# Performance work log

Hardware: AMD Instinct MI355X
Metric: run time of the kernel (lower is better)

## Reference

```python
import math
import jax, jax.numpy as jnp
import numpy as np

IMG = 512; P = 16; CIN = 3; COUT = 3; E = 768; NHEADS = 12; L = 8
NPH = IMG // P            # 32 patches per side
N = NPH * NPH             # 1024 tokens (must match learned 1024x1024 attn bias)
HD = E // NHEADS          # 64
INTER = min(E // 2, 128)  # 128, OutputProjection intermediate
EPS = 1e-5


def _sin_pe(n_h, n_w, d):
    # faithful port of get_2d_sinusoidal_encoding (second half stays zero)
    pe = np.zeros((n_h, n_w, d), dtype=np.float32)
    dq, dh = d // 4, d // 2
    div = np.exp(np.arange(0, dq, 2, dtype=np.float32) * (-math.log(10000.0) / dq))
    pr = np.arange(n_h, dtype=np.float32)[:, None]
    pc = np.arange(n_w, dtype=np.float32)[:, None]
    pe[:, :, 0:dq:2] = np.sin(pr * div)[:, None, :]
    pe[:, :, 1:dq:2] = np.cos(pr * div)[:, None, :]
    pe[:, :, dq:dh:2] = np.sin(pc * div)[None, :, :]
    pe[:, :, dq + 1:dh:2] = np.cos(pc * div)[None, :, :]
    return jnp.asarray(pe.reshape(-1, d))


def _ln(x, g, b):
    m = x.mean(-1, keepdims=True)
    v = ((x - m) ** 2).mean(-1, keepdims=True)
    return (x - m) * jax.lax.rsqrt(v + EPS) * g + b


def setup_inputs():
    key = jax.random.key(0)
    ks = iter(jax.random.split(key, 32))
    def nrm(shape, scale=0.02):
        return jax.random.normal(next(ks), shape, jnp.float32) * scale
    return {
        'x': jax.random.normal(next(ks), (2, CIN, IMG, IMG), jnp.float32),
        'conv_w': nrm((E, CIN, P, P)), 'conv_b': jnp.zeros((E,), jnp.float32),
        'ln1_g': jnp.ones((L, E), jnp.float32), 'ln1_b': jnp.zeros((L, E), jnp.float32),
        'qkv_w': nrm((L, 3 * E, E)),
        'proj_w': nrm((L, E, E)), 'proj_b': jnp.zeros((L, E), jnp.float32),
        'attn_bias': jax.random.normal(next(ks), (L, N, N), jnp.float32),  # torch.randn init
        'ln2_g': jnp.ones((L, E), jnp.float32), 'ln2_b': jnp.zeros((L, E), jnp.float32),
        'mlp_w1': nrm((L, 2 * E, E)), 'mlp_b1': jnp.zeros((L, 2 * E), jnp.float32),
        'mlp_w2': nrm((L, E, 2 * E)), 'mlp_b2': jnp.zeros((L, E), jnp.float32),
        'op_w1': nrm((INTER, E)), 'op_b1': jnp.zeros((INTER,), jnp.float32),
        'op_w2': nrm((P * P * COUT, INTER)), 'op_b2': jnp.zeros((P * P * COUT,), jnp.float32),
        'ag_wg': nrm((1, COUT), 0.2), 'ag_bng_w': jnp.ones((), jnp.float32), 'ag_bng_b': jnp.zeros((), jnp.float32),
        'ag_wx': nrm((1, CIN), 0.2), 'ag_bnx_w': jnp.ones((), jnp.float32), 'ag_bnx_b': jnp.zeros((), jnp.float32),
        'ag_psi_w': jnp.full((), 0.5, jnp.float32), 'ag_psi_b': jnp.zeros((), jnp.float32),
    }


def reference(x, conv_w, conv_b, ln1_g, ln1_b, qkv_w, proj_w, proj_b, attn_bias,
              ln2_g, ln2_b, mlp_w1, mlp_b1, mlp_w2, mlp_b2,
              op_w1, op_b1, op_w2, op_b2,
              ag_wg, ag_bng_w, ag_bng_b, ag_wx, ag_bnx_w, ag_bnx_b, ag_psi_w, ag_psi_b):
    B = x.shape[0]
    # --- VisionTransformerInput: patch-embed conv (stride == kernel) as reshape+GEMM ---
    xp = x.reshape(B, CIN, NPH, P, NPH, P).transpose(0, 2, 4, 1, 3, 5).reshape(B, N, CIN * P * P)
    t = xp @ conv_w.reshape(E, -1).T + conv_b
    t = t + _sin_pe(NPH, NPH, E)[None]

    # --- encoder blocks (scan over stacked per-layer params) ---
    def block(t, p):
        y = _ln(t, p['ln1_g'], p['ln1_b'])
        qkv = (y @ p['qkv_w'].T).reshape(B, N, 3, NHEADS, HD).transpose(2, 0, 3, 1, 4)
        q, k, v = qkv[0], qkv[1], qkv[2]
        s = jnp.einsum('bhnd,bhmd->bhnm', q, k) / math.sqrt(HD)
        # NOTE: relative_position_bias is computed but never added in the source (dead code);
        # only the learned (N,N) bias parameter is added.
        s = s + p['attn_bias'][None, None]
        a = jax.nn.softmax(s, axis=-1)
        o = jnp.einsum('bhnm,bhmd->bhnd', a, v).transpose(0, 2, 1, 3).reshape(B, N, E)
        o = o @ p['proj_w'].T + p['proj_b']
        t = t + (y + o)  # MHA has an extra internal residual (out = x + out) in the source
        h = _ln(t, p['ln2_g'], p['ln2_b'])
        h = jax.nn.gelu(h @ p['mlp_w1'].T + p['mlp_b1'], approximate=False) @ p['mlp_w2'].T + p['mlp_b2']
        return t + h, None

    stacked = {'ln1_g': ln1_g, 'ln1_b': ln1_b, 'qkv_w': qkv_w, 'proj_w': proj_w,
               'proj_b': proj_b, 'attn_bias': attn_bias, 'ln2_g': ln2_g, 'ln2_b': ln2_b,
               'mlp_w1': mlp_w1, 'mlp_b1': mlp_b1, 'mlp_w2': mlp_w2, 'mlp_b2': mlp_b2}
    t, _ = jax.lax.scan(block, t, stacked)

    # --- OutputProjection: MLP -> Fold -> attention gate -> (identity) interpolate ---
    h = jax.nn.relu(t @ op_w1.T + op_b1) @ op_w2.T + op_b2  # (B, N, C*P*P)
    # nn.Fold(kernel=stride=P): columns interpreted as (C, P, P)
    g = h.reshape(B, NPH, NPH, COUT, P, P).transpose(0, 3, 1, 4, 2, 5).reshape(B, COUT, IMG, IMG)
    inv = 1.0 / math.sqrt(1.0 + EPS)  # BatchNorm eval: running_mean=0, running_var=1
    g1 = jnp.einsum('bchw,oc->bohw', g, ag_wg) * (inv * ag_bng_w) + ag_bng_b
    x1 = jnp.einsum('bchw,oc->bohw', x, ag_wx) * (inv * ag_bnx_w) + ag_bnx_b
    psi = jax.nn.sigmoid(jax.nn.relu(g1 + x1) * ag_psi_w + ag_psi_b)
    out = g * (x * psi)  # x * att_gate's psi == skip_gated; then x_fold * skip_gated
    # F.interpolate to (output_size, output_size) with output_size == image_size: identity
    return out
```

## Files before the change

kernel.cpp:

```cpp
#include <hip/hip_runtime.h>
#include <math.h>

typedef unsigned short u16;
typedef unsigned int u32;
typedef __attribute__((ext_vector_type(8))) short bf16x8;
typedef __attribute__((ext_vector_type(16))) float f32x16;
typedef __attribute__((ext_vector_type(4))) float f4v;
typedef __attribute__((ext_vector_type(4))) u32 u32x4;

#define MFMA(a, b, c) __builtin_amdgcn_mfma_f32_32x32x16_bf16(a, b, c, 0, 0, 0)

#define SYNC_STEP() do {                                   \
    asm volatile("s_waitcnt vmcnt(0)" ::: "memory");       \
    __builtin_amdgcn_s_barrier();                          \
    __builtin_amdgcn_sched_barrier(0);                     \
} while (0)

#define SYNC_CNT6() do {                                   \
    asm volatile("s_waitcnt vmcnt(6)" ::: "memory");       \
    __builtin_amdgcn_s_barrier();                          \
    __builtin_amdgcn_sched_barrier(0);                     \
} while (0)

__device__ __forceinline__ float bf2f(u16 h) { return __uint_as_float(((u32)h) << 16); }

__device__ __forceinline__ void split2(float v, u16& h, u16& l) {
    u32 u = __float_as_uint(v);
    u32 hr = (u + 0x7FFFu + ((u >> 16) & 1u)) & 0xFFFF0000u;
    h = (u16)(hr >> 16);
    float lf = v - __uint_as_float(hr);
    u32 ul = __float_as_uint(lf);
    l = (u16)((ul + 0x7FFFu + ((ul >> 16) & 1u)) >> 16);
}

__device__ __forceinline__ u32 cvtpk(float lo, float hi) {
    u32 r;
    asm("v_cvt_pk_bf16_f32 %0, %1, %2" : "=v"(r) : "v"(lo), "v"(hi));
    return r;
}

__device__ __forceinline__ void swap32(u32& a, u32& b, int hi) {
    u32 ta = (u32)__shfl_xor((int)a, 32);
    u32 tb = (u32)__shfl_xor((int)b, 32);
    u32 na = hi ? tb : a;
    u32 nb = hi ? b : ta;
    a = na; b = nb;
}

__device__ __forceinline__ void repack(const f32x16& v, int base, int hi, bf16x8& fh, bf16x8& fl) {
    float p0 = v[base + 0], p1 = v[base + 1], p2 = v[base + 2], p3 = v[base + 3];
    float p4 = v[base + 4], p5 = v[base + 5], p6 = v[base + 6], p7 = v[base + 7];
    u32 X0 = cvtpk(p0, p1), X1 = cvtpk(p2, p3), X4 = cvtpk(p4, p5), X5 = cvtpk(p6, p7);
    float r0 = p0 - __uint_as_float(X0 << 16);
    float r1 = p1 - __uint_as_float(X0 & 0xFFFF0000u);
    float r2 = p2 - __uint_as_float(X1 << 16);
    float r3 = p3 - __uint_as_float(X1 & 0xFFFF0000u);
    float r4 = p4 - __uint_as_float(X4 << 16);
    float r5 = p5 - __uint_as_float(X4 & 0xFFFF0000u);
    float r6 = p6 - __uint_as_float(X5 << 16);
    float r7 = p7 - __uint_as_float(X5 & 0xFFFF0000u);
    u32 L0 = cvtpk(r0, r1), L1 = cvtpk(r2, r3), L4 = cvtpk(r4, r5), L5 = cvtpk(r6, r7);
    swap32(X0, X4, hi); swap32(X1, X5, hi);
    swap32(L0, L4, hi); swap32(L1, L5, hi);
    u32x4 th = {X0, X1, X4, X5};
    u32x4 tl = {L0, L1, L4, L5};
    fh = __builtin_bit_cast(bf16x8, th);
    fl = __builtin_bit_cast(bf16x8, tl);
}

__global__ __launch_bounds__(256) void pe_kernel(float* __restrict__ pe) {
    int idx = blockIdx.x * 256 + threadIdx.x;
    int n = idx / 768, d = idx - n * 768;
    float v = 0.0f;
    if (d < 384) {
// ... 46 lines not shown
    else if (idx < 2359296) { src = projw; off = idx - 1769472; }
    else if (idx < 3538944) { src = w1;    off = idx - 2359296; }
    else                    { src = w2;    off = idx - 3538944; }
    float4 v = *(const float4*)(src + off);
    split2(v.x, wh[idx], wl[idx]);
    split2(v.y, wh[idx + 1], wl[idx + 1]);
    split2(v.z, wh[idx + 2], wl[idx + 2]);
    split2(v.w, wh[idx + 3], wl[idx + 3]);
}

__global__ __launch_bounds__(256) void btrans(const float* __restrict__ src, float* __restrict__ dst) {
    __shared__ float tl[32][33];
    int bx = blockIdx.x & 31, by = blockIdx.x >> 5;
    int tx = threadIdx.x & 31, ty = threadIdx.x >> 5;
#pragma unroll
    for (int j = 0; j < 4; ++j)
        tl[ty + j * 8][tx] = src[(size_t)(by * 32 + ty + j * 8) * 1024 + bx * 32 + tx];
    __syncthreads();
#pragma unroll
    for (int j = 0; j < 4; ++j)
        dst[(size_t)(bx * 32 + ty + j * 8) * 1024 + by * 32 + tx] = tl[tx][ty + j * 8];
}

__global__ __launch_bounds__(256) void ln_kernel(const float* __restrict__ x,
                                                 const float* __restrict__ g,
                                                 const float* __restrict__ b,
                                                 u16* __restrict__ yh, u16* __restrict__ yl) {
    int row = blockIdx.x, tid = threadIdx.x;
    int wid = tid >> 6, lane = tid & 63;
    const float* xr = x + (size_t)row * 768;
    float v0 = xr[tid], v1 = xr[tid + 256], v2 = xr[tid + 512];
    __shared__ float ws[8];
    float sum = v0 + v1 + v2;
#pragma unroll
    for (int off = 32; off > 0; off >>= 1) sum += __shfl_xor(sum, off);
    if (lane == 0) ws[wid] = sum;
    __syncthreads();
    float mean = (ws[0] + ws[1] + ws[2] + ws[3]) * (1.0f / 768.0f);
    float d0 = v0 - mean, d1 = v1 - mean, d2 = v2 - mean;
    float vs = d0 * d0 + d1 * d1 + d2 * d2;
#pragma unroll
    for (int off = 32; off > 0; off >>= 1) vs += __shfl_xor(vs, off);
    if (lane == 0) ws[4 + wid] = vs;
    __syncthreads();
    float rstd = rsqrtf((ws[4] + ws[5] + ws[6] + ws[7]) * (1.0f / 768.0f) + 1e-5f);
    size_t o = (size_t)row * 768;
    split2(d0 * rstd * g[tid]       + b[tid],       yh[o + tid],       yl[o + tid]);
    split2(d1 * rstd * g[tid + 256] + b[tid + 256], yh[o + tid + 256], yl[o + tid + 256]);
    split2(d2 * rstd * g[tid + 512] + b[tid + 512], yh[o + tid + 512], yl[o + tid + 512]);
}

__device__ __forceinline__ int mrow(int r) { return (r + (r >> 2)) & 3; }

template <int MODE>
__global__ __launch_bounds__(256, 2) void gemm_sp(const u16* __restrict__ Ah, const u16* __restrict__ Al,
                                                  const u16* __restrict__ Bh, const u16* __restrict__ Bl,
                                                  const float* __restrict__ bias,
                                                  const float* __restrict__ res,
                                                  const float* __restrict__ auxf,
                                                  const u16* __restrict__ auxh, const u16* __restrict__ auxl,
                                                  float* __restrict__ C, u16* __restrict__ Ch, u16* __restrict__ Cl,
                                                  u16* __restrict__ Cth, u16* __restrict__ Ctl,
                                                  int M, int N, int K, int nby) {
    __shared__ u16 SH[36864];
    u16* As = SH;
    u16* Bs = SH + 12288;
    int tid = threadIdx.x;
    int wid = tid >> 6, lane = tid & 63;
    int hi = lane >> 5;
    int lq = lane & 31;
    int wm = wid >> 1, wn = wid & 1;

    int nwg = gridDim.x;
    int q8 = nwg >> 3;
    int swz = (blockIdx.x & 7) * q8 + (blockIdx.x >> 3);
    int cb = swz / nby, rb = swz - cb * nby;
    int m0 = rb * 64, n0 = cb * 128;

    f32x16 acc0 = {}, acc1 = {};

    auto stage = [&](int buf, int kt) {
#pragma unroll
        for (int c = 0; c < 2; ++c) {
            const u16* G = c ? Al : Ah;
            int row = wid * 16 + (lane >> 2);
            int ch = (lane & 3) ^ mrow(row);
            const u16* g = G + (size_t)(m0 + row) * K + kt + ch * 8;
            __builtin_amdgcn_global_load_lds((const __attribute__((address_space(1))) u32*)g,
                                             (__attribute__((address_space(3))) u32*)&As[(buf * 2 + c) * 2048 + (wid * 16) * 32],
                                             16, 0, 0);
        }
#pragma unroll
        for (int c = 0; c < 2; ++c) {
            const u16* G = c ? Bl : Bh;
#pragma unroll
            for (int j = 0; j < 2; ++j) {
                int row = wid * 32 + j * 16 + (lane >> 2);
                int ch = (lane & 3) ^ mrow(row);
                const u16* g = G + (size_t)(n0 + row) * K + kt + ch * 8;
                __builtin_amdgcn_global_load_lds((const __attribute__((address_space(1))) u32*)g,
                                                 (__attribute__((address_space(3))) u32*)&Bs[(buf * 2 + c) * 4096 + (wid * 32 + j * 16) * 32],
                                                 16, 0, 0);
            }
        }
    };

    int ar  = wm * 32 + lq;
    int br0 = wn * 64 + lq;
    int br1 = br0 + 32;

    auto compute = [&](int buf) {
#pragma unroll
        for (int kc = 0; kc < 2; ++kc) {
            int gc = (kc << 1) | hi;
            int oA  = ar  * 32 + ((gc ^ mrow(ar))  << 3);
            int oB0 = br0 * 32 + ((gc ^ mrow(br0)) << 3);
            int oB1 = br1 * 32 + ((gc ^ mrow(br1)) << 3);
            bf16x8 ah  = *(const bf16x8*)(As + (buf * 2 + 0) * 2048 + oA);
            bf16x8 al  = *(const bf16x8*)(As + (buf * 2 + 1) * 2048 + oA);
            bf16x8 b0h = *(const bf16x8*)(Bs + (buf * 2 + 0) * 4096 + oB0);
            bf16x8 b0l = *(const bf16x8*)(Bs + (buf * 2 + 1) * 4096 + oB0);
            bf16x8 b1h = *(const bf16x8*)(Bs + (buf * 2 + 0) * 4096 + oB1);
            bf16x8 b1l = *(const bf16x8*)(Bs + (buf * 2 + 1) * 4096 + oB1);
            acc0 = MFMA(ah, b0h, acc0);
            acc0 = MFMA(ah, b0l, acc0);
            acc0 = MFMA(al, b0h, acc0);
            acc1 = MFMA(ah, b1h, acc1);
            acc1 = MFMA(ah, b1l, acc1);
            acc1 = MFMA(al, b1h, acc1);
        }
    };

    int nk = K >> 5;
    stage(0, 0);
    stage(1, 32);
    int t = 0;
    for (; t < nk - 1; ++t) {
        SYNC_CNT6();
        if (t + 2 < nk) stage((t + 2) % 3, (t + 2) << 5);
        compute(t % 3);
    }
    SYNC_STEP();
    compute(t % 3);

    if (MODE == 7 && n0 >= 1536) {
        __syncthreads();
        auto scatterV = [&](const f32x16& a, int fn) {
            int c = wn * 64 + fn * 32 + lq;
            int rb2 = wm * 32 + (hi << 2);
#pragma unroll
            for (int r = 0; r < 16; ++r) {
                int rr = rb2 + (r & 3) + ((r >> 2) << 3);
                u16 hv, lv;
                split2(a[r], hv, lv);
                SH[c * 68 + rr] = hv;
                SH[8704 + c * 68 + rr] = lv;
            }
        };
        scatterV(acc0, 0);
        scatterV(acc1, 1);
        __syncthreads();
        int bb = m0 >> 10;
        int nbase = m0 & 1023;
#pragma unroll
        for (int pass = 0; pass < 4; ++pass) {
            int c2 = pass * 32 + (tid >> 3);
            int ch8 = tid & 7;
            int hcol = (n0 - 1536) + c2;
            int h2 = hcol >> 6, hd = hcol & 63;
            size_t dst = ((size_t)(bb * 12 + h2) * 64 + hd) * 1024 + nbase + ch8 * 8;
            int so = c2 * 68 + ch8 * 8;
            u32x4 ph = {*(const u32*)&SH[so], *(const u32*)&SH[so + 2],
                        *(const u32*)&SH[so + 4], *(const u32*)&SH[so + 6]};
            u32x4 pl = {*(const u32*)&SH[8704 + so], *(const u32*)&SH[8704 + so + 2],
                        *(const u32*)&SH[8704 + so + 4], *(const u32*)&SH[8704 + so + 6]};
            *(u32x4*)(Cth + dst) = ph;
            *(u32x4*)(Ctl + dst) = pl;
        }
        return;
    }

    auto epi = [&](const f32x16& a, int fn) {
        int col = n0 + wn * 64 + fn * 32 + lq;
        int rb2 = m0 + wm * 32 + (hi << 2);
#pragma unroll
        for (int r = 0; r < 16; ++r) {
            int row = rb2 + (r & 3) + ((r >> 2) << 3);
            float v = a[r];
            size_t o = (size_t)row * N + col;
            if (MODE == 1) C[o] = v + bias[col] + auxf[(size_t)(row & 1023) * N + col];
            else if (MODE == 2) C[o] = res[o] + (bf2f(auxh[o]) + bf2f(auxl[o])) + v + bias[col];
            else if (MODE == 3) {
                v += bias[col];
                v = 0.5f * v * (1.0f + erff(v * 0.70710678118654752f));
                split2(v, Ch[o], Cl[o]);
            }
            else if (MODE == 4) C[o] = res[o] + v + bias[col];
            else if (MODE == 5) {
                v += bias[col];
                v = fmaxf(v, 0.0f);
                split2(v, Ch[o], Cl[o]);
            }
            else if (MODE == 6) C[o] = v + bias[col];
            else if (MODE == 7) {
                size_t o7 = (size_t)row * 1536 + col;
                split2(v, Ch[o7], Cl[o7]);
            }
        }
    };
    epi(acc0, 0); epi(acc1, 1);
}

__global__ __launch_bounds__(256, 2) void attn_mfma(const u16* __restrict__ qh, const u16* __restrict__ ql,
                                                    const u16* __restrict__ vth, const u16* __restrict__ vtl,
                                                    const float* __restrict__ biasT,
                                                    u16* __restrict__ oh, u16* __restrict__ ol) {
    __shared__ u16 smem[2][2][4][2048];
    int tid = threadIdx.x;
    int wid = tid >> 6, lane = tid & 63;
    int s = wid & 1, p = wid >> 1;
    int lq = lane & 31;
    int hi = lane >> 5;
    int id = blockIdx.x;
    int xcd = id & 7;
    int j = id >> 3;
    int bh = xcd * 3 + (j >> 4);
    int qt = j & 15;
    int b = bh / 12, h = bh % 12;
    int bq0 = qt * 64;
    int gq = bq0 + s * 32 + lq;

    bf16x8 qfh[4], qfl[4];
    {
        size_t qo = (size_t)(b * 1024 + gq) * 1536 + h * 64 + hi * 8;
#pragma unroll
        for (int ks = 0; ks < 4; ++ks) {
            qfh[ks] = *(const bf16x8*)(qh + qo + ks * 16);
            qfl[ks] = *(const bf16x8*)(ql + qo + ks * 16);
        }
    }

    f32x16 oa = {}, ob = {};
    float m_i = -1e30f, l_i = 0.0f;

    auto stage = [&](int buf, int kb) {
        if (s == 0) {
#pragma unroll
            for (int c = 0; c < 2; ++c) {
                const u16* G = c ? ql : qh;
#pragma unroll
                for (int i = 0; i < 4; ++i) {
                    int r = 8 * i + (lane >> 3);
                    int cl = (lane & 7) ^ (r & 7);
                    const u16* g = G + (size_t)(b * 1024 + kb + r) * 1536 + 768 + h * 64 + cl * 8;
                    __builtin_amdgcn_global_load_lds((const __attribute__((address_space(1))) u32*)g,
                                                     (__attribute__((address_space(3))) u32*)&smem[p][buf][c][i * 512],
                                                     16, 0, 0);
                }
            }
        } else {
#pragma unroll
            for (int c = 0; c < 2; ++c) {
                const u16* G = c ? vtl : vth;
#pragma unroll
                for (int i = 0; i < 4; ++i) {
                    int r = 16 * i + (lane >> 2);
                    int cl = (lane & 3) ^ ((r >> 1) & 3);
                    const u16* g = G + ((size_t)(b * 12 + h) * 64 + r) * 1024 + kb + cl * 8;
                    __builtin_amdgcn_global_load_lds((const __attribute__((address_space(1))) u32*)g,
                                                     (__attribute__((address_space(3))) u32*)&smem[p][buf][2 + c][i * 512],
                                                     16, 0, 0);
                }
            }
        }
    };

    auto loadBias = [&](float (&bb)[16], int kb) {
        const float* bbase = biasT + (size_t)(kb + 4 * hi) * 1024 + gq;
#pragma unroll
        for (int g2 = 0; g2 < 4; ++g2)
#pragma unroll
            for (int q = 0; q < 4; ++q)
                bb[g2 * 4 + q] = bbase[(size_t)(g2 * 8 + q) * 1024];
    };

    auto compute = [&](int buf, const float (&bb)[16]) {
        const u16* Kh = &smem[p][buf][0][0];
        const u16* Kl = &smem[p][buf][1][0];
        const u16* Vh = &smem[p][buf][2][0];
        const u16* Vl = &smem[p][buf][3][0];
        f32x16 s0 = {}, s1 = {};
        __builtin_amdgcn_s_setprio(1);
#pragma unroll
        for (int ks = 0; ks < 2; ++ks) {
            int offA = lq * 64 + (((2 * ks + hi) ^ (lq & 7)) << 3);
            int offB = lq * 64 + (((2 * (ks + 2) + hi) ^ (lq & 7)) << 3);
            bf16x8 khA = *(const bf16x8*)(Kh + offA);
            bf16x8 klA = *(const bf16x8*)(Kl + offA);
            bf16x8 khB = *(const bf16x8*)(Kh + offB);
            bf16x8 klB = *(const bf16x8*)(Kl + offB);
            s0 = MFMA(khA, qfh[ks], s0);
            s1 = MFMA(khB, qfh[ks + 2], s1);
            s0 = MFMA(khA, qfl[ks], s0);
            s1 = MFMA(khB, qfl[ks + 2], s1);
            s0 = MFMA(klA, qfh[ks], s0);
            s1 = MFMA(klB, qfh[ks + 2], s1);
        }
        __builtin_amdgcn_s_setprio(0);
        bf16x8 vf[2][4];
#pragma unroll
        for (int kslot = 0; kslot < 2; ++kslot) {
            int offa = lq * 32 + (((2 * kslot + hi) ^ ((lq >> 1) & 3)) << 3);
            vf[kslot][0] = *(const bf16x8*)(Vh + offa);
            vf[kslot][1] = *(const bf16x8*)(Vh + offa + 1024);
            vf[kslot][2] = *(const bf16x8*)(Vl + offa);
            vf[kslot][3] = *(const bf16x8*)(Vl + offa + 1024);
        }
        f32x16 sa;
#pragma unroll
        for (int r = 0; r < 16; ++r) sa[r] = (s0[r] + s1[r]) * 0.125f + bb[r];
        float m01 = fmaxf(sa[0], sa[1]),  m23 = fmaxf(sa[2], sa[3]);
        float m45 = fmaxf(sa[4], sa[5]),  m67 = fmaxf(sa[6], sa[7]);
        float m89 = fmaxf(sa[8], sa[9]),  mab = fmaxf(sa[10], sa[11]);
        float mcd = fmaxf(sa[12], sa[13]), mef = fmaxf(sa[14], sa[15]);
        float pm = fmaxf(fmaxf(fmaxf(m01, m23), fmaxf(m45, m67)),
                         fmaxf(fmaxf(m89, mab), fmaxf(mcd, mef)));
        pm = fmaxf(pm, __shfl_xor(pm, 32));
        if (__any(pm > m_i + 8.0f)) {
            float mnew = fmaxf(m_i, pm);
            float scl = __expf(m_i - mnew);
            m_i = mnew;
            l_i *= scl;
#pragma unroll
            for (int r = 0; r < 16; ++r) {
                int qr = (r & 3) + 8 * (r >> 2) + 4 * hi;
                float fr = __shfl(scl, qr);
                oa[r] *= fr; ob[r] *= fr;
            }
        }
        float ls = 0.0f;
#pragma unroll
        for (int r = 0; r < 16; ++r) { sa[r] = __expf(sa[r] - m_i); ls += sa[r]; }
        ls += __shfl_xor(ls, 32);
        l_i += ls;
        __builtin_amdgcn_s_setprio(1);
#pragma unroll
        for (int kslot = 0; kslot < 2; ++kslot) {
            bf16x8 ph, pl;
            repack(sa, kslot * 8, hi, ph, pl);
            oa = MFMA(ph, vf[kslot][0], oa);
            oa = MFMA(ph, vf[kslot][2], oa);
            oa = MFMA(pl, vf[kslot][0], oa);
            ob = MFMA(ph, vf[kslot][1], ob);
            ob = MFMA(ph, vf[kslot][3], ob);
            ob = MFMA(pl, vf[kslot][1], ob);
        }
        __builtin_amdgcn_s_setprio(0);
    };

    float bbA[16], bbB[16];
    stage(0, p * 32);
    loadBias(bbA, p * 32);
    for (int ss = 0; ss < 16; ss += 2) {
        SYNC_STEP();
        if (ss + 1 < 16) { stage(1, (2 * (ss + 1) + p) * 32); loadBias(bbB, (2 * (ss + 1) + p) * 32); }
        compute(0, bbA);
        SYNC_STEP();
        if (ss + 2 < 16) { stage(0, (2 * (ss + 2) + p) * 32); loadBias(bbA, (2 * (ss + 2) + p) * 32); }
        compute(1, bbB);
    }
    __syncthreads();

    float* mlb = (float*)((char*)smem + 32768);
    mlb[((s * 2 + p) * 2 + 0) * 32 + lq] = m_i;
    mlb[((s * 2 + p) * 2 + 1) * 32 + lq] = l_i;
    __syncthreads();
    float mo  = mlb[((s * 2 + (p ^ 1)) * 2 + 0) * 32 + lq];
    float lo_ = mlb[((s * 2 + (p ^ 1)) * 2 + 1) * 32 + lq];
    float M = fmaxf(m_i, mo);
    float ea = __expf(m_i - M), eb = __expf(mo - M);
    float L = ea * l_i + eb * lo_;
    float f = ea / L;
    float frv[16];
#pragma unroll
    for (int r = 0; r < 16; ++r) frv[r] = __shfl(f, (r & 3) + 8 * (r >> 2) + 4 * hi);
    float* ox = (float*)((char*)smem + s * 8192);
    if (p == 1) {
#pragma unroll
        for (int r = 0; r < 16; ++r) {
            int qr = (r & 3) + 8 * (r >> 2) + 4 * hi;
            ox[qr * 64 + lq] = oa[r] * frv[r];
            ox[qr * 64 + 32 + lq] = ob[r] * frv[r];
        }
    }
    __syncthreads();
    if (p == 0) {
#pragma unroll
        for (int r = 0; r < 16; ++r) {
            int qr = (r & 3) + 8 * (r >> 2) + 4 * hi;
            float va = oa[r] * frv[r] + ox[qr * 64 + lq];
            float vb = ob[r] * frv[r] + ox[qr * 64 + 32 + lq];
            size_t d = (size_t)(b * 1024 + bq0 + s * 32 + qr) * 768 + h * 64;
            split2(va, oh[d + lq], ol[d + lq]);
            split2(vb, oh[d + 32 + lq], ol[d + 32 + lq]);
        }
    }
}

__global__ __launch_bounds__(256) void fold_gate(const float* __restrict__ hbuf,
                                                 const float* __restrict__ xin,
                                                 const float* __restrict__ wg,
                                                 const float* __restrict__ bngw,
                                                 const float* __restrict__ bngb,
                                                 const float* __restrict__ wx,
                                                 const float* __restrict__ bnxw,
                                                 const float* __restrict__ bnxb,
                                                 const float* __restrict__ psiw,
                                                 const float* __restrict__ psib,
                                                 float* __restrict__ out) {
    int idx = blockIdx.x * 256 + threadIdx.x;
// ... 24 lines not shown
    const float* x       = (const float*)d_in[0];
    const float* conv_w  = (const float*)d_in[1];
    const float* conv_b  = (const float*)d_in[2];
    const float* ln1_g   = (const float*)d_in[3];
    const float* ln1_b   = (const float*)d_in[4];
    const float* qkv_w   = (const float*)d_in[5];
    const float* proj_w  = (const float*)d_in[6];
    const float* proj_b  = (const float*)d_in[7];
    const float* attn_bs = (const float*)d_in[8];
    const float* ln2_g   = (const float*)d_in[9];
    const float* ln2_b   = (const float*)d_in[10];
    const float* mlp_w1  = (const float*)d_in[11];
    const float* mlp_b1  = (const float*)d_in[12];
    const float* mlp_w2  = (const float*)d_in[13];
    const float* mlp_b2  = (const float*)d_in[14];
    const float* op_w1   = (const float*)d_in[15];
    const float* op_b1   = (const float*)d_in[16];
    const float* op_w2   = (const float*)d_in[17];
    const float* op_b2   = (const float*)d_in[18];
    const float* ag_wg   = (const float*)d_in[19];
    const float* ag_bngw = (const float*)d_in[20];
    const float* ag_bngb = (const float*)d_in[21];
    const float* ag_wx   = (const float*)d_in[22];
    const float* ag_bnxw = (const float*)d_in[23];
    const float* ag_bnxb = (const float*)d_in[24];
    const float* ag_psiw = (const float*)d_in[25];
    const float* ag_psib = (const float*)d_in[26];
    float* out = (float*)d_out;

    char* w8 = (char*)d_ws;
    float* t     = (float*)(w8);
    u16* yh      = (u16*)(w8 + 6291456);
    u16* yl      = (u16*)(w8 + 9437184);
    u16* ath     = (u16*)(w8 + 12582912);
    u16* atl     = (u16*)(w8 + 15728640);
    u16* mh      = (u16*)(w8 + 18874368);
    u16* ml      = (u16*)(w8 + 25165824);
    u16* qh      = (u16*)(w8 + 31457280);
    u16* ql      = (u16*)(w8 + 37748736);
    u16* wh      = (u16*)(w8 + 44040192);
    u16* wl      = (u16*)(w8 + 53477376);
    float* biasT = (float*)(w8 + 62914560);
    float* pe  = (float*)qh;
    u16* xph = mh; u16* xpl = ml;
    u16* vth = mh; u16* vtl = ml;
    float* oph2 = (float*)qh;
    u16* o1h = ath; u16* o1l = atl;

    const size_t W_QKV = 0, W_PROJ = 1769472, W_MLP1 = 2359296, W_MLP2 = 3538944;

    pe_kernel<<<3072, 256, 0, stream>>>(pe);
    gather_kernel<<<6144, 256, 0, stream>>>(x, xph, xpl);
    fsplit<<<576, 256, 0, stream>>>(conv_w, wh, wl, 147456);
    gemm_sp<1><<<192, 256, 0, stream>>>(xph, xpl, wh, wl, conv_b, nullptr, pe,
                                        nullptr, nullptr, t, nullptr, nullptr,
                                        nullptr, nullptr, 2048, 768, 768, 32);

    for (int l = 0; l < 8; ++l) {
        wsplit_layer<<<4608, 256, 0, stream>>>(qkv_w + (size_t)l * 1769472, proj_w + (size_t)l * 589824,
                                               mlp_w1 + (size_t)l * 1179648, mlp_w2 + (size_t)l * 1179648,
                                               wh, wl);
        btrans<<<1024, 256, 0, stream>>>(attn_bs + (size_t)l * 1048576, biasT);
        ln_kernel<<<2048, 256, 0, stream>>>(t, ln1_g + l * 768, ln1_b + l * 768, yh, yl);
        gemm_sp<7><<<576, 256, 0, stream>>>(yh, yl, wh + W_QKV, wl + W_QKV, nullptr, nullptr,
                                            nullptr, nullptr, nullptr, nullptr, qh, ql,
                                            vth, vtl, 2048, 2304, 768, 32);
        attn_mfma<<<384, 256, 0, stream>>>(qh, ql, vth, vtl, biasT, ath, atl);
        gemm_sp<2><<<192, 256, 0, stream>>>(ath, atl, wh + W_PROJ, wl + W_PROJ, proj_b + l * 768,
                                            t, nullptr, yh, yl, t, nullptr, nullptr,
                                            nullptr, nullptr, 2048, 768, 768, 32);
        ln_kernel<<<2048, 256, 0, stream>>>(t, ln2_g + l * 768, ln2_b + l * 768, yh, yl);
        gemm_sp<3><<<384, 256, 0, stream>>>(yh, yl, wh + W_MLP1, wl + W_MLP1, mlp_b1 + l * 1536,
                                            nullptr, nullptr, nullptr, nullptr, nullptr, mh, ml,
                                            nullptr, nullptr, 2048, 1536, 768, 32);
        gemm_sp<4><<<192, 256, 0, stream>>>(mh, ml, wh + W_MLP2, wl + W_MLP2, mlp_b2 + l * 768,
                                            t, nullptr, nullptr, nullptr, t, nullptr, nullptr,
                                            nullptr, nullptr, 2048, 768, 1536, 32);
    }

    fsplit<<<1536, 256, 0, stream>>>(t, yh, yl, 393216);
    fsplit<<<96, 256, 0, stream>>>(op_w1, wh, wl, 24576);
    fsplit<<<96, 256, 0, stream>>>(op_w2, wh + 131072, wl + 131072, 24576);
    gemm_sp<5><<<32, 256, 0, stream>>>(yh, yl, wh, wl, op_b1, nullptr, nullptr,
                                       nullptr, nullptr, nullptr, o1h, o1l,
                                       nullptr, nullptr, 2048, 128, 768, 32);
    gemm_sp<6><<<192, 256, 0, stream>>>(o1h, o1l, wh + 131072, wl + 131072, op_b2, nullptr,
                                        nullptr, nullptr, nullptr, oph2, nullptr, nullptr,
                                        nullptr, nullptr, 2048, 768, 128, 32);
    fold_gate<<<2048, 256, 0, stream>>>(oph2, x, ag_wg, ag_bngw, ag_bngb,
                                        ag_wx, ag_bnxw, ag_bnxb, ag_psiw, ag_psib, out);
}
```

Baseline: 1.427 ms.

## Add 32-row GEMM tile variant, re-layout V staging, relax attention barrier waits

```diff
diff --git a/kernel.cpp b/kernel.cpp
--- a/kernel.cpp
+++ b/kernel.cpp
@@ -16,10 +16,10 @@
     __builtin_amdgcn_sched_barrier(0);                     \
 } while (0)
 
-#define SYNC_CNT6() do {                                   \
-    asm volatile("s_waitcnt vmcnt(6)" ::: "memory");       \
-    __builtin_amdgcn_s_barrier();                          \
-    __builtin_amdgcn_sched_barrier(0);                     \
+#define SYNC_CNT_LIT(nlit) do {                                    \
+    asm volatile("s_waitcnt vmcnt(" #nlit ")" ::: "memory");       \
+    __builtin_amdgcn_s_barrier();                                  \
+    __builtin_amdgcn_sched_barrier(0);                             \
 } while (0)
 
 __device__ __forceinline__ float bf2f(u16 h) { return __uint_as_float(((u32)h) << 16); }
@@ -172,7 +172,7 @@
 
 __device__ __forceinline__ int mrow(int r) { return (r + (r >> 2)) & 3; }
 
-template <int MODE>
+template <int MODE, int BM>
 __global__ __launch_bounds__(256, 2) void gemm_sp(const u16* __restrict__ Ah, const u16* __restrict__ Al,
                                                   const u16* __restrict__ Bh, const u16* __restrict__ Bl,
                                                   const float* __restrict__ bias,
@@ -182,32 +182,42 @@
                                                   float* __restrict__ C, u16* __restrict__ Ch, u16* __restrict__ Cl,
                                                   u16* __restrict__ Cth, u16* __restrict__ Ctl,
                                                   int M, int N, int K, int nby) {
-    __shared__ u16 SH[36864];
+    constexpr int ABUF = BM * 32;
+    __shared__ u16 SH[6 * ABUF + 24576];
     u16* As = SH;
-    u16* Bs = SH + 12288;
+    u16* Bs = SH + 6 * ABUF;
     int tid = threadIdx.x;
     int wid = tid >> 6, lane = tid & 63;
     int hi = lane >> 5;
     int lq = lane & 31;
-    int wm = wid >> 1, wn = wid & 1;
 
     int nwg = gridDim.x;
     int q8 = nwg >> 3;
     int swz = (blockIdx.x & 7) * q8 + (blockIdx.x >> 3);
     int cb = swz / nby, rb = swz - cb * nby;
-    int m0 = rb * 64, n0 = cb * 128;
+    int m0 = rb * BM, n0 = cb * 128;
 
     f32x16 acc0 = {}, acc1 = {};
 
     auto stage = [&](int buf, int kt) {
-#pragma unroll
-        for (int c = 0; c < 2; ++c) {
-            const u16* G = c ? Al : Ah;
-            int row = wid * 16 + (lane >> 2);
+        if constexpr (BM == 64) {
+#pragma unroll
+            for (int c = 0; c < 2; ++c) {
+                const u16* G = c ? Al : Ah;
+                int row = wid * 16 + (lane >> 2);
+                int ch = (lane & 3) ^ mrow(row);
+                const u16* g = G + (size_t)(m0 + row) * K + kt + ch * 8;
+                __builtin_amdgcn_global_load_lds((const __attribute__((address_space(1))) u32*)g,
+                                                 (__attribute__((address_space(3))) u32*)&As[(buf * 2 + c) * ABUF + (wid * 16) * 32],
+                                                 16, 0, 0);
+            }
+        } else {
+            const u16* G = (wid & 1) ? Al : Ah;
+            int row = (wid >> 1) * 16 + (lane >> 2);
             int ch = (lane & 3) ^ mrow(row);
             const u16* g = G + (size_t)(m0 + row) * K + kt + ch * 8;
             __builtin_amdgcn_global_load_lds((const __attribute__((address_space(1))) u32*)g,
-                                             (__attribute__((address_space(3))) u32*)&As[(buf * 2 + c) * 2048 + (wid * 16) * 32],
+                                             (__attribute__((address_space(3))) u32*)&As[(buf * 2 + (wid & 1)) * ABUF + ((wid >> 1) * 16) * 32],
                                              16, 0, 0);
         }
 #pragma unroll
@@ -225,8 +235,8 @@
         }
     };
 
-    int ar  = wm * 32 + lq;
-    int br0 = wn * 64 + lq;
+    int ar  = (BM == 64) ? ((wid >> 1) * 32 + lq) : lq;
+    int br0 = (BM == 64) ? ((wid & 1) * 64 + lq) : (wid * 32 + lq);
     int br1 = br0 + 32;
 
     auto compute = [&](int buf) {
@@ -235,19 +245,21 @@
             int gc = (kc << 1) | hi;
             int oA  = ar  * 32 + ((gc ^ mrow(ar))  << 3);
             int oB0 = br0 * 32 + ((gc ^ mrow(br0)) << 3);
-            int oB1 = br1 * 32 + ((gc ^ mrow(br1)) << 3);
-            bf16x8 ah  = *(const bf16x8*)(As + (buf * 2 + 0) * 2048 + oA);
-            bf16x8 al  = *(const bf16x8*)(As + (buf * 2 + 1) * 2048 + oA);
+            bf16x8 ah  = *(const bf16x8*)(As + (buf * 2 + 0) * ABUF + oA);
+            bf16x8 al  = *(const bf16x8*)(As + (buf * 2 + 1) * ABUF + oA);
             bf16x8 b0h = *(const bf16x8*)(Bs + (buf * 2 + 0) * 4096 + oB0);
             bf16x8 b0l = *(const bf16x8*)(Bs + (buf * 2 + 1) * 4096 + oB0);
-            bf16x8 b1h = *(const bf16x8*)(Bs + (buf * 2 + 0) * 4096 + oB1);
-            bf16x8 b1l = *(const bf16x8*)(Bs + (buf * 2 + 1) * 4096 + oB1);
             acc0 = MFMA(ah, b0h, acc0);
             acc0 = MFMA(ah, b0l, acc0);
             acc0 = MFMA(al, b0h, acc0);
-            acc1 = MFMA(ah, b1h, acc1);
-            acc1 = MFMA(ah, b1l, acc1);
-            acc1 = MFMA(al, b1h, acc1);
+            if constexpr (BM == 64) {
+                int oB1 = br1 * 32 + ((gc ^ mrow(br1)) << 3);
+                bf16x8 b1h = *(const bf16x8*)(Bs + (buf * 2 + 0) * 4096 + oB1);
+                bf16x8 b1l = *(const bf16x8*)(Bs + (buf * 2 + 1) * 4096 + oB1);
+                acc1 = MFMA(ah, b1h, acc1);
+                acc1 = MFMA(ah, b1l, acc1);
+                acc1 = MFMA(al, b1h, acc1);
+            }
         }
     };
 
@@ -256,53 +268,55 @@
     stage(1, 32);
     int t = 0;
     for (; t < nk - 1; ++t) {
-        SYNC_CNT6();
+        if constexpr (BM == 64) SYNC_CNT_LIT(6); else SYNC_CNT_LIT(5);
         if (t + 2 < nk) stage((t + 2) % 3, (t + 2) << 5);
         compute(t % 3);
     }
     SYNC_STEP();
     compute(t % 3);
 
-    if (MODE == 7 && n0 >= 1536) {
-        __syncthreads();
-        auto scatterV = [&](const f32x16& a, int fn) {
-            int c = wn * 64 + fn * 32 + lq;
-            int rb2 = wm * 32 + (hi << 2);
-#pragma unroll
-            for (int r = 0; r < 16; ++r) {
-                int rr = rb2 + (r & 3) + ((r >> 2) << 3);
-                u16 hv, lv;
-                split2(a[r], hv, lv);
-                SH[c * 68 + rr] = hv;
-                SH[8704 + c * 68 + rr] = lv;
-            }
-        };
-        scatterV(acc0, 0);
-        scatterV(acc1, 1);
-        __syncthreads();
-        int bb = m0 >> 10;
-        int nbase = m0 & 1023;
-#pragma unroll
-        for (int pass = 0; pass < 4; ++pass) {
-            int c2 = pass * 32 + (tid >> 3);
-            int ch8 = tid & 7;
-            int hcol = (n0 - 1536) + c2;
-            int h2 = hcol >> 6, hd = hcol & 63;
-            size_t dst = ((size_t)(bb * 12 + h2) * 64 + hd) * 1024 + nbase + ch8 * 8;
-            int so = c2 * 68 + ch8 * 8;
-            u32x4 ph = {*(const u32*)&SH[so], *(const u32*)&SH[so + 2],
-                        *(const u32*)&SH[so + 4], *(const u32*)&SH[so + 6]};
-            u32x4 pl = {*(const u32*)&SH[8704 + so], *(const u32*)&SH[8704 + so + 2],
-                        *(const u32*)&SH[8704 + so + 4], *(const u32*)&SH[8704 + so + 6]};
-            *(u32x4*)(Cth + dst) = ph;
-            *(u32x4*)(Ctl + dst) = pl;
-        }
-        return;
-    }
-
-    auto epi = [&](const f32x16& a, int fn) {
-        int col = n0 + wn * 64 + fn * 32 + lq;
-        int rb2 = m0 + wm * 32 + (hi << 2);
+    if constexpr (MODE == 7) {
+        if (n0 >= 1536) {
+            __syncthreads();
+            auto scatterV = [&](const f32x16& a, int fn) {
+                int c = (wid & 1) * 64 + fn * 32 + lq;
+                int rb2 = (wid >> 1) * 32 + (hi << 2);
+#pragma unroll
+                for (int r = 0; r < 16; ++r) {
+                    int rr = rb2 + (r & 3) + ((r >> 2) << 3);
+                    u16 hv, lv;
+                    split2(a[r], hv, lv);
+                    SH[c * 68 + rr] = hv;
+                    SH[8704 + c * 68 + rr] = lv;
+                }
+            };
+            scatterV(acc0, 0);
+            scatterV(acc1, 1);
+            __syncthreads();
+            int bb = m0 >> 10;
+            int nbase = m0 & 1023;
+#pragma unroll
+            for (int pass = 0; pass < 4; ++pass) {
+                int c2 = pass * 32 + (tid >> 3);
+                int ch8 = tid & 7;
+                int hcol = (n0 - 1536) + c2;
+                int h2 = hcol >> 6, hd = hcol & 63;
+                size_t dst = ((size_t)(bb * 12 + h2) * 64 + hd) * 1024 + nbase + ch8 * 8;
+                int so = c2 * 68 + ch8 * 8;
+                u32x4 ph = {*(const u32*)&SH[so], *(const u32*)&SH[so + 2],
+                            *(const u32*)&SH[so + 4], *(const u32*)&SH[so + 6]};
+                u32x4 pl = {*(const u32*)&SH[8704 + so], *(const u32*)&SH[8704 + so + 2],
+                            *(const u32*)&SH[8704 + so + 4], *(const u32*)&SH[8704 + so + 6]};
+                *(u32x4*)(Cth + dst) = ph;
+                *(u32x4*)(Ctl + dst) = pl;
+            }
+            return;
+        }
+    }
+
+    auto epi = [&](const f32x16& a, int ncol) {
+        int col = n0 + ncol + lq;
+        int rb2 = m0 + ((BM == 64) ? ((wid >> 1) * 32) : 0) + (hi << 2);
 #pragma unroll
         for (int r = 0; r < 16; ++r) {
             int row = rb2 + (r & 3) + ((r >> 2) << 3);
@@ -328,7 +342,12 @@
             }
         }
     };
-    epi(acc0, 0); epi(acc1, 1);
+    if constexpr (BM == 64) {
+        epi(acc0, (wid & 1) * 64);
+        epi(acc1, (wid & 1) * 64 + 32);
+    } else {
+        epi(acc0, wid * 32);
+    }
 }
 
 __global__ __launch_bounds__(256, 2) void attn_mfma(const u16* __restrict__ qh, const u16* __restrict__ ql,
@@ -349,6 +368,7 @@
     int b = bh / 12, h = bh % 12;
     int bq0 = qt * 64;
     int gq = bq0 + s * 32 + lq;
+    size_t vbase = (size_t)(b * 12 + h) * 65536;
 
     bf16x8 qfh[4], qfl[4];
     {
@@ -384,9 +404,12 @@
                 const u16* G = c ? vtl : vth;
 #pragma unroll
                 for (int i = 0; i < 4; ++i) {
-                    int r = 16 * i + (lane >> 2);
-                    int cl = (lane & 3) ^ ((r >> 1) & 3);
-                    const u16* g = G + ((size_t)(b * 12 + h) * 64 + r) * 1024 + kb + cl * 8;
+                    int r = 8 * i + (lane >> 3);
+                    int pc = lane & 7;
+                    int lc = pc ^ (r & 7);
+                    int hd = r + ((lc >> 2) << 5);
+                    int kc = lc & 3;
+                    const u16* g = G + vbase + (size_t)hd * 1024 + kb + kc * 8;
                     __builtin_amdgcn_global_load_lds((const __attribute__((address_space(1))) u32*)g,
                                                      (__attribute__((address_space(3))) u32*)&smem[p][buf][2 + c][i * 512],
                                                      16, 0, 0);
@@ -430,11 +453,13 @@
         bf16x8 vf[2][4];
 #pragma unroll
         for (int kslot = 0; kslot < 2; ++kslot) {
-            int offa = lq * 32 + (((2 * kslot + hi) ^ ((lq >> 1) & 3)) << 3);
-            vf[kslot][0] = *(const bf16x8*)(Vh + offa);
-            vf[kslot][1] = *(const bf16x8*)(Vh + offa + 1024);
-            vf[kslot][2] = *(const bf16x8*)(Vl + offa);
-            vf[kslot][3] = *(const bf16x8*)(Vl + offa + 1024);
+            int ks2 = 2 * kslot + hi;
+            int off0 = lq * 64 + ((ks2 ^ (lq & 7)) << 3);
+            int off1 = lq * 64 + (((4 + ks2) ^ (lq & 7)) << 3);
+            vf[kslot][0] = *(const bf16x8*)(Vh + off0);
+            vf[kslot][1] = *(const bf16x8*)(Vh + off1);
+            vf[kslot][2] = *(const bf16x8*)(Vl + off0);
+            vf[kslot][3] = *(const bf16x8*)(Vl + off1);
         }
         f32x16 sa;
 #pragma unroll
@@ -482,10 +507,10 @@
     stage(0, p * 32);
     loadBias(bbA, p * 32);
     for (int ss = 0; ss < 16; ss += 2) {
-        SYNC_STEP();
+        SYNC_CNT_LIT(16);
         if (ss + 1 < 16) { stage(1, (2 * (ss + 1) + p) * 32); loadBias(bbB, (2 * (ss + 1) + p) * 32); }
         compute(0, bbA);
-        SYNC_STEP();
+        SYNC_CNT_LIT(16);
         if (ss + 2 < 16) { stage(0, (2 * (ss + 2) + p) * 32); loadBias(bbA, (2 * (ss + 2) + p) * 32); }
         compute(1, bbB);
     }
@@ -616,9 +641,9 @@
     pe_kernel<<<3072, 256, 0, stream>>>(pe);
     gather_kernel<<<6144, 256, 0, stream>>>(x, xph, xpl);
     fsplit<<<576, 256, 0, stream>>>(conv_w, wh, wl, 147456);
-    gemm_sp<1><<<192, 256, 0, stream>>>(xph, xpl, wh, wl, conv_b, nullptr, pe,
-                                        nullptr, nullptr, t, nullptr, nullptr,
-                                        nullptr, nullptr, 2048, 768, 768, 32);
+    gemm_sp<1, 32><<<384, 256, 0, stream>>>(xph, xpl, wh, wl, conv_b, nullptr, pe,
+                                            nullptr, nullptr, t, nullptr, nullptr,
+                                            nullptr, nullptr, 2048, 768, 768, 64);
 
     for (int l = 0; l < 8; ++l) {
         wsplit_layer<<<4608, 256, 0, stream>>>(qkv_w + (size_t)l * 1769472, proj_w + (size_t)l * 589824,
@@ -626,31 +651,31 @@
                                                wh, wl);
         btrans<<<1024, 256, 0, stream>>>(attn_bs + (size_t)l * 1048576, biasT);
         ln_kernel<<<2048, 256, 0, stream>>>(t, ln1_g + l * 768, ln1_b + l * 768, yh, yl);
-        gemm_sp<7><<<576, 256, 0, stream>>>(yh, yl, wh + W_QKV, wl + W_QKV, nullptr, nullptr,
-                                            nullptr, nullptr, nullptr, nullptr, qh, ql,
-                                            vth, vtl, 2048, 2304, 768, 32);
+        gemm_sp<7, 64><<<576, 256, 0, stream>>>(yh, yl, wh + W_QKV, wl + W_QKV, nullptr, nullptr,
+                                                nullptr, nullptr, nullptr, nullptr, qh, ql,
+                                                vth, vtl, 2048, 2304, 768, 32);
         attn_mfma<<<384, 256, 0, stream>>>(qh, ql, vth, vtl, biasT, ath, atl);
-        gemm_sp<2><<<192, 256, 0, stream>>>(ath, atl, wh + W_PROJ, wl + W_PROJ, proj_b + l * 768,
-                                            t, nullptr, yh, yl, t, nullptr, nullptr,
-                                            nullptr, nullptr, 2048, 768, 768, 32);
+        gemm_sp<2, 32><<<384, 256, 0, stream>>>(ath, atl, wh + W_PROJ, wl + W_PROJ, proj_b + l * 768,
+                                                t, nullptr, yh, yl, t, nullptr, nullptr,
+                                                nullptr, nullptr, 2048, 768, 768, 64);
         ln_kernel<<<2048, 256, 0, stream>>>(t, ln2_g + l * 768, ln2_b + l * 768, yh, yl);
-        gemm_sp<3><<<384, 256, 0, stream>>>(yh, yl, wh + W_MLP1, wl + W_MLP1, mlp_b1 + l * 1536,
-                                            nullptr, nullptr, nullptr, nullptr, nullptr, mh, ml,
-                                            nullptr, nullptr, 2048, 1536, 768, 32);
-        gemm_sp<4><<<192, 256, 0, stream>>>(mh, ml, wh + W_MLP2, wl + W_MLP2, mlp_b2 + l * 768,
-                                            t, nullptr, nullptr, nullptr, t, nullptr, nullptr,
-                                            nullptr, nullptr, 2048, 768, 1536, 32);
+        gemm_sp<3, 64><<<384, 256, 0, stream>>>(yh, yl, wh + W_MLP1, wl + W_MLP1, mlp_b1 + l * 1536,
+                                                nullptr, nullptr, nullptr, nullptr, nullptr, mh, ml,
+                                                nullptr, nullptr, 2048, 1536, 768, 32);
+        gemm_sp<4, 32><<<384, 256, 0, stream>>>(mh, ml, wh + W_MLP2, wl + W_MLP2, mlp_b2 + l * 768,
+                                                t, nullptr, nullptr, nullptr, t, nullptr, nullptr,
+                                                nullptr, nullptr, 2048, 768, 1536, 64);
     }
 
     fsplit<<<1536, 256, 0, stream>>>(t, yh, yl, 393216);
     fsplit<<<96, 256, 0, stream>>>(op_w1, wh, wl, 24576);
     fsplit<<<96, 256, 0, stream>>>(op_w2, wh + 131072, wl + 131072, 24576);
-    gemm_sp<5><<<32, 256, 0, stream>>>(yh, yl, wh, wl, op_b1, nullptr, nullptr,
-                                       nullptr, nullptr, nullptr, o1h, o1l,
-                                       nullptr, nullptr, 2048, 128, 768, 32);
-    gemm_sp<6><<<192, 256, 0, stream>>>(o1h, o1l, wh + 131072, wl + 131072, op_b2, nullptr,
-                                        nullptr, nullptr, nullptr, oph2, nullptr, nullptr,
-                                        nullptr, nullptr, 2048, 768, 128, 32);
+    gemm_sp<5, 32><<<64, 256, 0, stream>>>(yh, yl, wh, wl, op_b1, nullptr, nullptr,
+                                           nullptr, nullptr, nullptr, o1h, o1l,
+                                           nullptr, nullptr, 2048, 128, 768, 64);
+    gemm_sp<6, 32><<<384, 256, 0, stream>>>(o1h, o1l, wh + 131072, wl + 131072, op_b2, nullptr,
+                                            nullptr, nullptr, nullptr, oph2, nullptr, nullptr,
+                                            nullptr, nullptr, 2048, 768, 128, 64);
     fold_gate<<<2048, 256, 0, stream>>>(oph2, x, ag_wg, ag_bngw, ag_bngb,
                                         ag_wx, ag_bnxw, ag_bnxb, ag_psiw, ag_psib, out);
 }
```

Measured after the change: 1.520 ms. +6.5%, slower.

## Add 128x128-tile split-bf16 GEMM for QKV and MLP1 projections

Applied to the files above, without the earlier changes.

```diff
diff --git a/kernel.cpp b/kernel.cpp
--- a/kernel.cpp
+++ b/kernel.cpp
@@ -16,10 +16,10 @@
     __builtin_amdgcn_sched_barrier(0);                     \
 } while (0)
 
-#define SYNC_CNT6() do {                                   \
-    asm volatile("s_waitcnt vmcnt(6)" ::: "memory");       \
-    __builtin_amdgcn_s_barrier();                          \
-    __builtin_amdgcn_sched_barrier(0);                     \
+#define SYNC_CNT_LIT(nlit) do {                                    \
+    asm volatile("s_waitcnt vmcnt(" #nlit ")" ::: "memory");       \
+    __builtin_amdgcn_s_barrier();                                  \
+    __builtin_amdgcn_sched_barrier(0);                             \
 } while (0)
 
 __device__ __forceinline__ float bf2f(u16 h) { return __uint_as_float(((u32)h) << 16); }
@@ -180,7 +180,6 @@
                                                   const float* __restrict__ auxf,
                                                   const u16* __restrict__ auxh, const u16* __restrict__ auxl,
                                                   float* __restrict__ C, u16* __restrict__ Ch, u16* __restrict__ Cl,
-                                                  u16* __restrict__ Cth, u16* __restrict__ Ctl,
                                                   int M, int N, int K, int nby) {
     __shared__ u16 SH[36864];
     u16* As = SH;
@@ -189,7 +188,6 @@
     int wid = tid >> 6, lane = tid & 63;
     int hi = lane >> 5;
     int lq = lane & 31;
-    int wm = wid >> 1, wn = wid & 1;
 
     int nwg = gridDim.x;
     int q8 = nwg >> 3;
@@ -225,8 +223,8 @@
         }
     };
 
-    int ar  = wm * 32 + lq;
-    int br0 = wn * 64 + lq;
+    int ar  = (wid >> 1) * 32 + lq;
+    int br0 = (wid & 1) * 64 + lq;
     int br1 = br0 + 32;
 
     auto compute = [&](int buf) {
@@ -256,53 +254,16 @@
     stage(1, 32);
     int t = 0;
     for (; t < nk - 1; ++t) {
-        SYNC_CNT6();
+        SYNC_CNT_LIT(6);
         if (t + 2 < nk) stage((t + 2) % 3, (t + 2) << 5);
         compute(t % 3);
     }
     SYNC_STEP();
     compute(t % 3);
 
-    if (MODE == 7 && n0 >= 1536) {
-        __syncthreads();
-        auto scatterV = [&](const f32x16& a, int fn) {
-            int c = wn * 64 + fn * 32 + lq;
-            int rb2 = wm * 32 + (hi << 2);
-#pragma unroll
-            for (int r = 0; r < 16; ++r) {
-                int rr = rb2 + (r & 3) + ((r >> 2) << 3);
-                u16 hv, lv;
-                split2(a[r], hv, lv);
-                SH[c * 68 + rr] = hv;
-                SH[8704 + c * 68 + rr] = lv;
-            }
-        };
-        scatterV(acc0, 0);
-        scatterV(acc1, 1);
-        __syncthreads();
-        int bb = m0 >> 10;
-        int nbase = m0 & 1023;
-#pragma unroll
-        for (int pass = 0; pass < 4; ++pass) {
-            int c2 = pass * 32 + (tid >> 3);
-            int ch8 = tid & 7;
-            int hcol = (n0 - 1536) + c2;
-            int h2 = hcol >> 6, hd = hcol & 63;
-            size_t dst = ((size_t)(bb * 12 + h2) * 64 + hd) * 1024 + nbase + ch8 * 8;
-            int so = c2 * 68 + ch8 * 8;
-            u32x4 ph = {*(const u32*)&SH[so], *(const u32*)&SH[so + 2],
-                        *(const u32*)&SH[so + 4], *(const u32*)&SH[so + 6]};
-            u32x4 pl = {*(const u32*)&SH[8704 + so], *(const u32*)&SH[8704 + so + 2],
-                        *(const u32*)&SH[8704 + so + 4], *(const u32*)&SH[8704 + so + 6]};
-            *(u32x4*)(Cth + dst) = ph;
-            *(u32x4*)(Ctl + dst) = pl;
-        }
-        return;
-    }
-
-    auto epi = [&](const f32x16& a, int fn) {
-        int col = n0 + wn * 64 + fn * 32 + lq;
-        int rb2 = m0 + wm * 32 + (hi << 2);
+    auto epi = [&](const f32x16& a, int ncol) {
+        int col = n0 + ncol + lq;
+        int rb2 = m0 + (wid >> 1) * 32 + (hi << 2);
 #pragma unroll
         for (int r = 0; r < 16; ++r) {
             int row = rb2 + (r & 3) + ((r >> 2) << 3);
@@ -310,11 +271,6 @@
             size_t o = (size_t)row * N + col;
             if (MODE == 1) C[o] = v + bias[col] + auxf[(size_t)(row & 1023) * N + col];
             else if (MODE == 2) C[o] = res[o] + (bf2f(auxh[o]) + bf2f(auxl[o])) + v + bias[col];
-            else if (MODE == 3) {
-                v += bias[col];
-                v = 0.5f * v * (1.0f + erff(v * 0.70710678118654752f));
-                split2(v, Ch[o], Cl[o]);
-            }
             else if (MODE == 4) C[o] = res[o] + v + bias[col];
             else if (MODE == 5) {
                 v += bias[col];
@@ -322,13 +278,155 @@
                 split2(v, Ch[o], Cl[o]);
             }
             else if (MODE == 6) C[o] = v + bias[col];
-            else if (MODE == 7) {
+        }
+    };
+    epi(acc0, (wid & 1) * 64);
+    epi(acc1, (wid & 1) * 64 + 32);
+}
+
+template <int MODE>
+__global__ __launch_bounds__(256, 2) void gemm_sq(const u16* __restrict__ Ah, const u16* __restrict__ Al,
+                                                  const u16* __restrict__ Bh, const u16* __restrict__ Bl,
+                                                  const float* __restrict__ bias,
+                                                  u16* __restrict__ Ch, u16* __restrict__ Cl,
+                                                  u16* __restrict__ Cth, u16* __restrict__ Ctl,
+                                                  int M, int N, int K, int nby) {
+    __shared__ u16 SH[32768];
+    int tid = threadIdx.x;
+    int wid = tid >> 6, lane = tid & 63;
+    int hi = lane >> 5;
+    int lq = lane & 31;
+    int wm = wid >> 1, wn = wid & 1;
+
+    int nwg = gridDim.x;
+    int q8 = nwg >> 3;
+    int swz = (blockIdx.x & 7) * q8 + (blockIdx.x >> 3);
+    int cb = swz / nby, rb = swz - cb * nby;
+    int m0 = rb * 128, n0 = cb * 128;
+
+    f32x16 acc00 = {}, acc01 = {}, acc10 = {}, acc11 = {};
+
+    const u16* srcs[4] = {Ah, Al, Bh, Bl};
+    auto stage = [&](int buf, int kt) {
+        const u16* G = srcs[wid];
+        int rbase = (wid < 2) ? m0 : n0;
+#pragma unroll
+        for (int i = 0; i < 8; ++i) {
+            int row = i * 16 + (lane >> 2);
+            int ch = (lane & 3) ^ mrow(row);
+            const u16* g = G + (size_t)(rbase + row) * K + kt + ch * 8;
+            __builtin_amdgcn_global_load_lds((const __attribute__((address_space(1))) u32*)g,
+                                             (__attribute__((address_space(3))) u32*)&SH[buf * 16384 + wid * 4096 + i * 512],
+                                             16, 0, 0);
+        }
+    };
+
+    int ar0 = wm * 64 + lq, ar1 = ar0 + 32;
+    int br0 = wn * 64 + lq, br1 = br0 + 32;
+
+    auto compute = [&](int buf) {
+        const u16* SAh = SH + buf * 16384;
+        const u16* SAl = SAh + 4096;
+        const u16* SBh = SAl + 4096;
+        const u16* SBl = SBh + 4096;
+#pragma unroll
+        for (int kc = 0; kc < 2; ++kc) {
+            int gc = (kc << 1) | hi;
+            int oA0 = ar0 * 32 + ((gc ^ mrow(ar0)) << 3);
+            int oA1 = ar1 * 32 + ((gc ^ mrow(ar1)) << 3);
+            int oB0 = br0 * 32 + ((gc ^ mrow(br0)) << 3);
+            int oB1 = br1 * 32 + ((gc ^ mrow(br1)) << 3);
+            bf16x8 a0h = *(const bf16x8*)(SAh + oA0);
+            bf16x8 a0l = *(const bf16x8*)(SAl + oA0);
+            bf16x8 a1h = *(const bf16x8*)(SAh + oA1);
+            bf16x8 a1l = *(const bf16x8*)(SAl + oA1);
+            bf16x8 b0h = *(const bf16x8*)(SBh + oB0);
+            bf16x8 b0l = *(const bf16x8*)(SBl + oB0);
+            bf16x8 b1h = *(const bf16x8*)(SBh + oB1);
+            bf16x8 b1l = *(const bf16x8*)(SBl + oB1);
+            acc00 = MFMA(a0h, b0h, acc00);
+            acc00 = MFMA(a0h, b0l, acc00);
+            acc00 = MFMA(a0l, b0h, acc00);
+            acc01 = MFMA(a0h, b1h, acc01);
+            acc01 = MFMA(a0h, b1l, acc01);
+            acc01 = MFMA(a0l, b1h, acc01);
+            acc10 = MFMA(a1h, b0h, acc10);
+            acc10 = MFMA(a1h, b0l, acc10);
+            acc10 = MFMA(a1l, b0h, acc10);
+            acc11 = MFMA(a1h, b1h, acc11);
+            acc11 = MFMA(a1h, b1l, acc11);
+            acc11 = MFMA(a1l, b1h, acc11);
+        }
+    };
+
+    int nk = K >> 5;
+    stage(0, 0);
+    for (int t = 0; t < nk; ++t) {
+        SYNC_STEP();
+        if (t + 1 < nk) stage((t + 1) & 1, (t + 1) << 5);
+        compute(t & 1);
+    }
+
+    if (MODE == 7 && n0 >= 1536) {
+        int bb = m0 >> 10;
+        int nbase = m0 & 1023;
+#pragma unroll
+        for (int P = 0; P < 2; ++P) {
+            __syncthreads();
+            if (wm == P) {
+                auto scat = [&](const f32x16& a, int fm, int fn) {
+                    int c = wn * 64 + fn * 32 + lq;
+                    int rbl = fm * 32 + (hi << 2);
+#pragma unroll
+                    for (int r = 0; r < 16; ++r) {
+                        int rr = rbl + (r & 3) + ((r >> 2) << 3);
+                        u16 hv, lv;
+                        split2(a[r], hv, lv);
+                        SH[c * 68 + rr] = hv;
+                        SH[8704 + c * 68 + rr] = lv;
+                    }
+                };
+                scat(acc00, 0, 0); scat(acc01, 0, 1); scat(acc10, 1, 0); scat(acc11, 1, 1);
+            }
+            __syncthreads();
+#pragma unroll
+            for (int pass = 0; pass < 4; ++pass) {
+                int c2 = pass * 32 + (tid >> 3);
+                int ch8 = tid & 7;
+                int hcol = (n0 - 1536) + c2;
+                int h2 = hcol >> 6, hd = hcol & 63;
+                size_t dst = ((size_t)(bb * 12 + h2) * 64 + hd) * 1024 + nbase + P * 64 + ch8 * 8;
+                int so = c2 * 68 + ch8 * 8;
+                u32x4 ph = {*(const u32*)&SH[so], *(const u32*)&SH[so + 2],
+                            *(const u32*)&SH[so + 4], *(const u32*)&SH[so + 6]};
+                u32x4 pl = {*(const u32*)&SH[8704 + so], *(const u32*)&SH[8704 + so + 2],
+                            *(const u32*)&SH[8704 + so + 4], *(const u32*)&SH[8704 + so + 6]};
+                *(u32x4*)(Cth + dst) = ph;
+                *(u32x4*)(Ctl + dst) = pl;
+            }
+        }
+        return;
+    }
+
+    auto epi = [&](const f32x16& a, int fm, int fn) {
+        int col = n0 + wn * 64 + fn * 32 + lq;
+        int rb2 = m0 + wm * 64 + fm * 32 + (hi << 2);
+#pragma unroll
+        for (int r = 0; r < 16; ++r) {
+            int row = rb2 + (r & 3) + ((r >> 2) << 3);
+            float v = a[r];
+            if (MODE == 3) {
+                size_t o = (size_t)row * N + col;
+                v += bias[col];
+                v = 0.5f * v * (1.0f + erff(v * 0.70710678118654752f));
+                split2(v, Ch[o], Cl[o]);
+            } else if (MODE == 7) {
                 size_t o7 = (size_t)row * 1536 + col;
                 split2(v, Ch[o7], Cl[o7]);
             }
         }
     };
-    epi(acc0, 0); epi(acc1, 1);
+    epi(acc00, 0, 0); epi(acc01, 0, 1); epi(acc10, 1, 0); epi(acc11, 1, 1);
 }
 
 __global__ __launch_bounds__(256, 2) void attn_mfma(const u16* __restrict__ qh, const u16* __restrict__ ql,
@@ -617,8 +715,7 @@
     gather_kernel<<<6144, 256, 0, stream>>>(x, xph, xpl);
     fsplit<<<576, 256, 0, stream>>>(conv_w, wh, wl, 147456);
     gemm_sp<1><<<192, 256, 0, stream>>>(xph, xpl, wh, wl, conv_b, nullptr, pe,
-                                        nullptr, nullptr, t, nullptr, nullptr,
-                                        nullptr, nullptr, 2048, 768, 768, 32);
+                                        nullptr, nullptr, t, nullptr, nullptr, 2048, 768, 768, 32);
 
     for (int l = 0; l < 8; ++l) {
         wsplit_layer<<<4608, 256, 0, stream>>>(qkv_w + (size_t)l * 1769472, proj_w + (size_t)l * 589824,
@@ -626,31 +723,27 @@
                                                wh, wl);
         btrans<<<1024, 256, 0, stream>>>(attn_bs + (size_t)l * 1048576, biasT);
         ln_kernel<<<2048, 256, 0, stream>>>(t, ln1_g + l * 768, ln1_b + l * 768, yh, yl);
-        gemm_sp<7><<<576, 256, 0, stream>>>(yh, yl, wh + W_QKV, wl + W_QKV, nullptr, nullptr,
-                                            nullptr, nullptr, nullptr, nullptr, qh, ql,
-                                            vth, vtl, 2048, 2304, 768, 32);
+        gemm_sq<7><<<288, 256, 0, stream>>>(yh, yl, wh + W_QKV, wl + W_QKV, nullptr,
+                                            qh, ql, vth, vtl, 2048, 2304, 768, 16);
         attn_mfma<<<384, 256, 0, stream>>>(qh, ql, vth, vtl, biasT, ath, atl);
         gemm_sp<2><<<192, 256, 0, stream>>>(ath, atl, wh + W_PROJ, wl + W_PROJ, proj_b + l * 768,
-                                            t, nullptr, yh, yl, t, nullptr, nullptr,
-                                            nullptr, nullptr, 2048, 768, 768, 32);
+                                            t, nullptr, yh, yl, t, nullptr, nullptr, 2048, 768, 768, 32);
         ln_kernel<<<2048, 256, 0, stream>>>(t, ln2_g + l * 768, ln2_b + l * 768, yh, yl);
-        gemm_sp<3><<<384, 256, 0, stream>>>(yh, yl, wh + W_MLP1, wl + W_MLP1, mlp_b1 + l * 1536,
-                                            nullptr, nullptr, nullptr, nullptr, nullptr, mh, ml,
-                                            nullptr, nullptr, 2048, 1536, 768, 32);
+        gemm_sq<3><<<192, 256, 0, stream>>>(yh, yl, wh + W_MLP1, wl + W_MLP1, mlp_b1 + l * 1536,
+                                            mh, ml, nullptr, nullptr, 2048, 1536, 768, 16);
         gemm_sp<4><<<192, 256, 0, stream>>>(mh, ml, wh + W_MLP2, wl + W_MLP2, mlp_b2 + l * 768,
                                             t, nullptr, nullptr, nullptr, t, nullptr, nullptr,
-                                            nullptr, nullptr, 2048, 768, 1536, 32);
+                                            2048, 768, 1536, 32);
     }
 
     fsplit<<<1536, 256, 0, stream>>>(t, yh, yl, 393216);
     fsplit<<<96, 256, 0, stream>>>(op_w1, wh, wl, 24576);
     fsplit<<<96, 256, 0, stream>>>(op_w2, wh + 131072, wl + 131072, 24576);
     gemm_sp<5><<<32, 256, 0, stream>>>(yh, yl, wh, wl, op_b1, nullptr, nullptr,
-                                       nullptr, nullptr, nullptr, o1h, o1l,
-                                       nullptr, nullptr, 2048, 128, 768, 32);
+                                       nullptr, nullptr, nullptr, o1h, o1l, 2048, 128, 768, 32);
     gemm_sp<6><<<192, 256, 0, stream>>>(o1h, o1l, wh + 131072, wl + 131072, op_b2, nullptr,
                                         nullptr, nullptr, nullptr, oph2, nullptr, nullptr,
-                                        nullptr, nullptr, 2048, 768, 128, 32);
+                                        2048, 768, 128, 32);
     fold_gate<<<2048, 256, 0, stream>>>(oph2, x, ag_wg, ag_bngw, ag_bngb,
                                         ag_wx, ag_bnxw, ag_bnxb, ag_psiw, ag_psib, out);
 }
```

Result: no change. 1.403 ms (-1.7%).
